# Kernel optimization log

Measured on AMD Instinct MI355X. Metric: run time of the kernel, lower is better.

Reference implementation:

```python
import jax, jax.numpy as jnp
import numpy as np

ALPHA = 0.2  # LeakyReLU negative slope
EPS = 1e-16


def setup_inputs() -> dict:
    key = jax.random.key(0)
    k0, k1, k2, k3 = jax.random.split(key, 4)
    N, E, F_in, F_out, HEADS = 50000, 1600000, 256, 128, 4
    H = jax.random.normal(k0, (N, F_in), dtype=jnp.float32)
    edge_index = jax.random.randint(k1, (2, E), 0, N)  # row0=src, row1=dst
    # Xavier-ish scaled params
    W = jax.random.normal(k2, (HEADS, F_out, F_in), dtype=jnp.float32) * (1.0 / np.sqrt(F_in))
    a = jax.random.normal(k3, (HEADS, 2 * F_out), dtype=jnp.float32) * 0.1
    bias = jnp.zeros((F_out,), dtype=jnp.float32)
    return {"H": H, "edge_index": edge_index, "W": W, "a": a, "bias": bias}


def reference(H, edge_index, W, a, bias):
    """GAT layer: per-head edge attention + segment softmax over src + SpMM, mean over heads.

    H: [N, F_in]; edge_index: [2, E]; W: [heads, F_out, F_in]; a: [heads, 2*F_out]; bias: [F_out]
    Note: a(concat(h_src, h_dst)) == h_src @ a[:F_out] + h_dst @ a[F_out:], so we compute the
    two per-node scores once on nodes instead of materializing the E x 2*F_out concat.
    """
    N = H.shape[0]
    heads, F_out, _ = W.shape
    src, dst = edge_index[0], edge_index[1]
    outs = []
    for h in range(heads):
        Ht = H @ W[h].T                      # [N, F_out]
        s_src = Ht @ a[h, :F_out]            # [N]
        s_dst = Ht @ a[h, F_out:]            # [N]
        e = s_src[src] + s_dst[dst]          # [E]
        e = jnp.where(e > 0, e, ALPHA * e)   # LeakyReLU
        # segment softmax over src nodes (matches scatter amax + scatter_add)
        e_max = jax.ops.segment_max(e, src, num_segments=N)    # [N], -inf for isolated nodes
        e_exp = jnp.exp(e - e_max[src])                         # [E]
        denom = jax.ops.segment_sum(e_exp, src, num_segments=N) # [N]
        attn = e_exp / (denom[src] + EPS)                       # [E]
        # sparse.mm(attention, Ht): out[i] = sum_{(i,j) in E} attn_ij * Ht[j]
        out = jax.ops.segment_sum(attn[:, None] * Ht[dst], src, num_segments=N)  # [N, F_out]
        outs.append(out)
    final = jnp.mean(jnp.stack(outs, axis=0), axis=0) + bias
    return final
```

## Files before the change

### kernel.cpp

```cpp
#include <hip/hip_runtime.h>

#define ALPHA 0.2f
#define EPS 1e-16f

static constexpr int F_IN = 256;
static constexpr int F_OUT = 128;
static constexpr int HEADS = 4;
static constexpr int COLS = HEADS * F_OUT;

typedef __bf16 bf16x8 __attribute__((ext_vector_type(8)));
typedef float f32x4 __attribute__((ext_vector_type(4)));

static __device__ __forceinline__ unsigned short f2bf(float f) {
  unsigned int u = __float_as_uint(f);
  unsigned int r = (u + 0x7FFFu + ((u >> 16) & 1u)) >> 16;
  return (unsigned short)r;
}
static __device__ __forceinline__ float bf_lo(unsigned int u) {
  return __uint_as_float(u << 16);
}
static __device__ __forceinline__ float bf_hi(unsigned int u) {
  return __uint_as_float(u & 0xFFFF0000u);
}
static __device__ __forceinline__ void cvt8(const float4& p0, const float4& p1, bf16x8& v) {
  v[0] = (__bf16)p0.x; v[1] = (__bf16)p0.y; v[2] = (__bf16)p0.z; v[3] = (__bf16)p0.w;
  v[4] = (__bf16)p1.x; v[5] = (__bf16)p1.y; v[6] = (__bf16)p1.z; v[7] = (__bf16)p1.w;
}

__global__ __launch_bounds__(256) void k_gemm_q(const float* __restrict__ A,
                                                const float* __restrict__ Wf,
                                                unsigned char* __restrict__ Hq,
                                                unsigned char* __restrict__ rec,
                                                float* __restrict__ ssrc,
                                                const float* __restrict__ Av, int N, int Tg,
                                                const int* __restrict__ src,
                                                int* __restrict__ cnt,
                                                unsigned short* __restrict__ rank, int E) {
  if ((int)blockIdx.x >= Tg) {
    int i = ((int)blockIdx.x - Tg) * 256 + threadIdx.x;
    const int stride = 1024 * 256;
    for (; i < E; i += stride) rank[i] = (unsigned short)atomicAdd(&cnt[src[i]], 1);
    return;
  }
  __shared__ __bf16 As[128][40];
  __shared__ __bf16 Bs[128][40];
  __shared__ float sS[128], sD[128];
  const int q8 = Tg >> 3, r8 = Tg & 7;
  const int xcd = blockIdx.x & 7, ii = blockIdx.x >> 3;
  const int gp = (xcd < r8) ? xcd * (q8 + 1) + ii
                            : r8 * (q8 + 1) + (xcd - r8) * q8 + ii;
  const int by = gp >> 2;
  const int bx = gp & 3;
  const int t = threadIdx.x;
  const int w = t >> 6, l = t & 63;
  const int wr = w >> 1, wc = w & 1;
  const int m0 = by << 7, n0 = bx << 7;
  const int lr = t >> 1, seg16 = (t & 1) << 4;
  int ar = m0 + lr; if (ar >= N) ar = N - 1;
  const float* Ap = A + (size_t)ar * F_IN + seg16;
  const float* Wp = Wf + (size_t)(n0 + lr) * F_IN + seg16;
  f32x4 acc[4][4] = {};
  for (int k0 = 0; k0 < F_IN; k0 += 32) {
    const float4 f0 = *(const float4*)(Ap + k0);
    const float4 f1 = *(const float4*)(Ap + k0 + 4);
    const float4 f2 = *(const float4*)(Ap + k0 + 8);
    const float4 f3 = *(const float4*)(Ap + k0 + 12);
    const float4 g0 = *(const float4*)(Wp + k0);
    const float4 g1 = *(const float4*)(Wp + k0 + 4);
    const float4 g2 = *(const float4*)(Wp + k0 + 8);
    const float4 g3 = *(const float4*)(Wp + k0 + 12);
    bf16x8 v0, v1, u0, u1;
    cvt8(f0, f1, v0); cvt8(f2, f3, v1);
    cvt8(g0, g1, u0); cvt8(g2, g3, u1);
    __syncthreads();
    *(bf16x8*)&As[lr][seg16] = v0;  *(bf16x8*)&As[lr][seg16 + 8] = v1;
    *(bf16x8*)&Bs[lr][seg16] = u0;  *(bf16x8*)&Bs[lr][seg16 + 8] = u1;
    __syncthreads();
    const int kb = (l >> 4) << 3;
    bf16x8 af[4], bf_[4];
#pragma unroll
    for (int mi = 0; mi < 4; ++mi)
      af[mi] = *(const bf16x8*)&As[(wr << 6) + (mi << 4) + (l & 15)][kb];
#pragma unroll
    for (int ni = 0; ni < 4; ++ni)
      bf_[ni] = *(const bf16x8*)&Bs[(wc << 6) + (ni << 4) + (l & 15)][kb];
#pragma unroll
    for (int mi = 0; mi < 4; ++mi)
#pragma unroll
      for (int ni = 0; ni < 4; ++ni)
        acc[mi][ni] = __builtin_amdgcn_mfma_f32_16x16x32_bf16(af[mi], bf_[ni], acc[mi][ni], 0, 0, 0);
  }
  {
    float as_[4], ad_[4];
#pragma unroll
    for (int ni = 0; ni < 4; ++ni) {
      const int f = (wc << 6) + (ni << 4) + (l & 15);
      as_[ni] = Av[bx * 256 + f];
      ad_[ni] = Av[bx * 256 + 128 + f];
    }
#pragma unroll
    for (int mi = 0; mi < 4; ++mi)
#pragma unroll
      for (int r = 0; r < 4; ++r) {
        float ds_ = 0.f, dd_ = 0.f;
#pragma unroll
        for (int ni = 0; ni < 4; ++ni) {
          ds_ = fmaf(acc[mi][ni][r], as_[ni], ds_);
          dd_ = fmaf(acc[mi][ni][r], ad_[ni], dd_);
        }
#pragma unroll
        for (int m = 1; m < 16; m <<= 1) {
          ds_ += __shfl_xor(ds_, m);
          dd_ += __shfl_xor(dd_, m);
        }
        if (wc == 0 && (l & 15) == 0) {
          const int rl = (wr << 6) + (mi << 4) + ((l >> 4) << 2) + r;
          sS[rl] = ds_; sD[rl] = dd_;
        }
      }
    __syncthreads();
    if (wc == 1) {
#pragma unroll
      for (int mi = 0; mi < 4; ++mi)
#pragma unroll
        for (int r = 0; r < 4; ++r) {
          float ds_ = 0.f, dd_ = 0.f;
#pragma unroll
          for (int ni = 0; ni < 4; ++ni) {
            ds_ = fmaf(acc[mi][ni][r], as_[ni], ds_);
            dd_ = fmaf(acc[mi][ni][r], ad_[ni], dd_);
          }
#pragma unroll
          for (int m = 1; m < 16; m <<= 1) {
            ds_ += __shfl_xor(ds_, m);
            dd_ += __shfl_xor(dd_, m);
          }
          if ((l & 15) == 0) {
            const int rl = (wr << 6) + (mi << 4) + ((l >> 4) << 2) + r;
            const int row = m0 + rl;
            if (row < N) {
              ssrc[row * 4 + bx] = sS[rl] + ds_;
              *(float*)&rec[(size_t)row * 32 + (bx << 2)] = sD[rl] + dd_;
            }
          }
        }
    }
  }
  const int bxg = (bx << 1) + wc;
#pragma unroll
  for (int mi = 0; mi < 4; ++mi)
#pragma unroll
    for (int r = 0; r < 4; ++r) {
      float mx = 0.f;
#pragma unroll
      for (int ni = 0; ni < 4; ++ni) mx = fmaxf(mx, fabsf(acc[mi][ni][r]));
#pragma unroll
      for (int m = 1; m < 16; m <<= 1) mx = fmaxf(mx, __shfl_xor(mx, m));
      const int row = m0 + (wr << 6) + (mi << 4) + ((l >> 4) << 2) + r;
      if (row < N) {
        const float inv = (mx > 0.f) ? 127.f / mx : 0.f;
        if ((l & 15) == 0)
          *(unsigned short*)&rec[(size_t)row * 32 + 16 + (bxg << 1)] = f2bf(mx * (1.f / 127.f));
        unsigned int pk = 0;
#pragma unroll
        for (int ni = 0; ni < 4; ++ni) {
          float tq = fminf(fmaxf(rintf(acc[mi][ni][r] * inv), -127.f), 127.f);
          pk |= ((unsigned int)(((int)tq + 128) & 255)) << (8 * ni);
        }
        *(unsigned int*)&Hq[(size_t)row * 512 + (bxg << 6) + ((l & 15) << 2)] = pk;
      }
    }
}

__global__ __launch_bounds__(1024) void k_scan1(int* __restrict__ cnt,
                                                int* __restrict__ bsum, int N) {
  __shared__ int ws[16];
  const int t = threadIdx.x, g = blockIdx.x * 1024 + t;
  const int lane = t & 63, w = t >> 6;
  int v = (g < N) ? cnt[g] : 0;
#pragma unroll
  for (int o = 1; o < 64; o <<= 1) {
    const int y = __shfl_up(v, o);
    if (lane >= o) v += y;
  }
  if (lane == 63) ws[w] = v;
  __syncthreads();
  if (w == 0) {
    int s = (lane < 16) ? ws[lane] : 0;
#pragma unroll
    for (int o = 1; o < 16; o <<= 1) {
      const int y = __shfl_up(s, o);
      if (lane >= o) s += y;
    }
    if (lane < 16) ws[lane] = s;
  }
  __syncthreads();
  v += (w > 0) ? ws[w - 1] : 0;
  if (g < N) cnt[g] = v;
  if (t == 1023) bsum[blockIdx.x] = v;
}

__global__ __launch_bounds__(1024) void k_scan3(const int* __restrict__ part,
                                                const int* __restrict__ bsum,
                                                int* __restrict__ off, int N, int nb) {
  __shared__ int sbuf[256];
  const int t = threadIdx.x;
  if (t < 64) {
    int carry = 0;
    for (int base = 0; base < nb; base += 64) {
      int v = (base + t < nb) ? bsum[base + t] : 0;
#pragma unroll
      for (int o = 1; o < 64; o <<= 1) {
        const int y = __shfl_up(v, o);
        if (t >= o) v += y;
      }
      v += carry;
      if (base + t < nb) sbuf[base + t] = v;
      carry = __shfl(v, 63);
    }
  }
  __syncthreads();
  const int g = blockIdx.x * 1024 + t;
  if (g == 0) off[0] = 0;
  if (g < N) off[g + 1] = part[g] + (blockIdx.x ? sbuf[blockIdx.x - 1] : 0);
}

__global__ void k_scatter(const int* __restrict__ src, const int* __restrict__ dst,
                          const int* __restrict__ off, const unsigned short* __restrict__ rank,
                          unsigned short* __restrict__ csr_dst, int E) {
  int i = blockIdx.x * blockDim.x + threadIdx.x;
  const int stride = gridDim.x * blockDim.x;
  for (; i < E; i += stride)
    csr_dst[off[src[i]] + rank[i]] = (unsigned short)dst[i];
}

__global__ __launch_bounds__(256) void k_spmm(const uint2* __restrict__ Hq2,
    const float4* __restrict__ ssrc4, const unsigned char* __restrict__ rec,
    const int* __restrict__ off, const unsigned short* __restrict__ csr_dst,
    const float* __restrict__ bias, float* __restrict__ out, int N) {
  __shared__ float wbuf[4][8][72];
  __shared__ int   ibuf[4][64];
  const int wv = threadIdx.x >> 6;
  const int lane = threadIdx.x & 63;
  const int n = (blockIdx.x << 2) + wv;
  if (n >= N) return;
  const int hg = lane >> 4;
  const int b8 = lane >> 3;
  const float4 ss4 = ssrc4[n];
  float den4[4] = {};
  float acc[8] = {};
  float sw = 0.f;
  const int beg = off[n], end = off[n + 1];
  for (int c0 = beg; c0 < end; c0 += 64) {
    const int cnt = min(64, end - c0);
    if (lane < cnt) {
      const int d = csr_dst[c0 + lane];
      ibuf[wv][lane] = d << 6;
      const float4 sd4 = *(const float4*)&rec[(size_t)d * 32];
      const uint4  sc  = *(const uint4*)&rec[(size_t)d * 32 + 16];
      float e0 = ss4.x + sd4.x; e0 = fmaxf(e0, ALPHA * e0);
      float e1 = ss4.y + sd4.y; e1 = fmaxf(e1, ALPHA * e1);
      float e2 = ss4.z + sd4.z; e2 = fmaxf(e2, ALPHA * e2);
      float e3 = ss4.w + sd4.w; e3 = fmaxf(e3, ALPHA * e3);
      const float w0 = __expf(e0), w1 = __expf(e1), w2 = __expf(e2), w3 = __expf(e3);
      den4[0] += w0; den4[1] += w1; den4[2] += w2; den4[3] += w3;
      wbuf[wv][0][lane] = w0 * bf_lo(sc.x); wbuf[wv][1][lane] = w0 * bf_hi(sc.x);
      wbuf[wv][2][lane] = w1 * bf_lo(sc.y); wbuf[wv][3][lane] = w1 * bf_hi(sc.y);
      wbuf[wv][4][lane] = w2 * bf_lo(sc.z); wbuf[wv][5][lane] = w2 * bf_hi(sc.z);
      wbuf[wv][6][lane] = w3 * bf_lo(sc.w); wbuf[wv][7][lane] = w3 * bf_hi(sc.w);
    }
#pragma unroll 8
    for (int j = 0; j < cnt; ++j) {
      const float wgt = wbuf[wv][b8][j];
      const int db = ibuf[wv][j];
      const uint2 q = Hq2[db + lane];
      sw += wgt;
      acc[0] = fmaf(wgt, (float)(q.x & 0xffu),         acc[0]);
      acc[1] = fmaf(wgt, (float)((q.x >> 8) & 0xffu),  acc[1]);
      acc[2] = fmaf(wgt, (float)((q.x >> 16) & 0xffu), acc[2]);
      acc[3] = fmaf(wgt, (float)(q.x >> 24),           acc[3]);
      acc[4] = fmaf(wgt, (float)(q.y & 0xffu),         acc[4]);
      acc[5] = fmaf(wgt, (float)((q.y >> 8) & 0xffu),  acc[5]);
      acc[6] = fmaf(wgt, (float)((q.y >> 16) & 0xffu), acc[6]);
      acc[7] = fmaf(wgt, (float)(q.y >> 24),           acc[7]);
    }
  }
#pragma unroll
  for (int k = 0; k < 4; ++k)
#pragma unroll
    for (int m = 1; m < 64; m <<= 1) den4[k] += __shfl_xor(den4[k], m);
  const float r = 1.f / (den4[hg] + EPS);
  const float corr = 128.f * sw;
#pragma unroll
  for (int i = 0; i < 8; ++i) acc[i] = (acc[i] - corr) * r;
#pragma unroll
  for (int i = 0; i < 8; ++i) {
    acc[i] += __shfl_xor(acc[i], 16);
    acc[i] += __shfl_xor(acc[i], 32);
  }
  if (lane < 16) {
    const int base = ((lane >> 3) & 1) * 64 + ((lane & 7) << 1);
#pragma unroll
    for (int k = 0; k < 4; ++k) {
      const float2 b2 = *(const float2*)&bias[base + k * 16];
      *(float2*)&out[(size_t)n * F_OUT + base + k * 16] =
          make_float2(0.25f * acc[k] + b2.x, 0.25f * acc[k + 4] + b2.y);
    }
  }
}

extern "C" void kernel_launch(void* const* d_in, const int* in_sizes, int n_in,
                              void* d_out, int out_size, void* d_ws, size_t ws_size,
                              hipStream_t stream) {
  const float* H    = (const float*)d_in[0];
  const int*   ei   = (const int*)d_in[1];
  const float* W    = (const float*)d_in[2];
  const float* a    = (const float*)d_in[3];
  const float* bias = (const float*)d_in[4];
  const int N = in_sizes[0] / F_IN;
  const int E = in_sizes[1] / 2;
  const int* src = ei;
  const int* dst = ei + E;

  char* ws = (char*)d_ws;
  size_t o = 0;
  auto alloc = [&](size_t bytes) -> void* {
    void* p = ws + o;
    o = (o + bytes + 255) & ~(size_t)255;
    return p;
  };
  unsigned char*  Hq  = (unsigned char*)alloc((size_t)N * COLS);
  float* ssrc = (float*)alloc((size_t)N * HEADS * sizeof(float));
  unsigned char* rec = (unsigned char*)alloc((size_t)N * 32);
  int*   cnt  = (int*)alloc((size_t)N * sizeof(int));
  int*   off  = (int*)alloc(((size_t)N + 1) * sizeof(int));
  unsigned short* csr = (unsigned short*)alloc((size_t)E * sizeof(unsigned short));
  unsigned short* rank = (unsigned short*)alloc((size_t)E * sizeof(unsigned short));
  const int nb = (N + 1023) / 1024;
  int*   bsum = (int*)alloc((size_t)nb * sizeof(int));

  hipMemsetAsync(cnt, 0, (size_t)N * sizeof(int), stream);

  const int nb128 = (N + 127) / 128;
  const int Tg = 4 * nb128;
  k_gemm_q<<<Tg + 1024, 256, 0, stream>>>(H, W, Hq, rec, ssrc, a, N, Tg,
                                          src, cnt, rank, E);
  k_scan1<<<nb, 1024, 0, stream>>>(cnt, bsum, N);
  k_scan3<<<nb, 1024, 0, stream>>>(cnt, bsum, off, N, nb);
  k_scatter<<<1024, 256, 0, stream>>>(src, dst, off, rank, csr, E);
  k_spmm<<<(N + 3) / 4, 256, 0, stream>>>((const uint2*)Hq, (const float4*)ssrc,
                                          rec, off, csr, bias, (float*)d_out, N);
}
```

Measured before the change: 290.1 us.

## Replace global-atomic CSR build with LDS-binned counting split across GEMM-overlapped launches

Global atomics used for per-edge rank counting are replaced by LDS-binned histograms: 64 edge chunks × 4 source ranges, with 16-bit packed counters. A per-chunk base-offset table is built, and a placement kernel then assigns CSR slots using LDS atomics. The GEMM tiles are split into four slices, and each slice is co-launched with one CSR-build phase (histogram, local scan, block scan, base computation) so the GEMM hides that latency. This drops the memset, the rank array and the scattered global atomics. In exchange it adds bcnt/base tables of size 64×N, extra passes over src, and a 16-bit per-bin count limit.

```diff
diff --git a/kernel.cpp b/kernel.cpp
--- a/kernel.cpp
+++ b/kernel.cpp
@@ -7,6 +7,7 @@
 static constexpr int F_OUT = 128;
 static constexpr int HEADS = 4;
 static constexpr int COLS = HEADS * F_OUT;
+static constexpr int NCH = 64;
 
 typedef __bf16 bf16x8 __attribute__((ext_vector_type(8)));
 typedef float f32x4 __attribute__((ext_vector_type(4)));
@@ -27,99 +28,75 @@
   v[4] = (__bf16)p1.x; v[5] = (__bf16)p1.y; v[6] = (__bf16)p1.z; v[7] = (__bf16)p1.w;
 }
 
-__global__ __launch_bounds__(256) void k_gemm_q(const float* __restrict__ A,
-                                                const float* __restrict__ Wf,
-                                                unsigned char* __restrict__ Hq,
-                                                unsigned char* __restrict__ rec,
-                                                float* __restrict__ ssrc,
-                                                const float* __restrict__ Av, int N, int Tg,
-                                                const int* __restrict__ src,
-                                                int* __restrict__ cnt,
-                                                unsigned short* __restrict__ rank, int E) {
-  if ((int)blockIdx.x >= Tg) {
-    int i = ((int)blockIdx.x - Tg) * 256 + threadIdx.x;
-    const int stride = 1024 * 256;
-    for (; i < E; i += stride) rank[i] = (unsigned short)atomicAdd(&cnt[src[i]], 1);
-    return;
-  }
-  __shared__ __bf16 As[128][40];
-  __shared__ __bf16 Bs[128][40];
-  __shared__ float sS[128], sD[128];
-  const int q8 = Tg >> 3, r8 = Tg & 7;
-  const int xcd = blockIdx.x & 7, ii = blockIdx.x >> 3;
-  const int gp = (xcd < r8) ? xcd * (q8 + 1) + ii
-                            : r8 * (q8 + 1) + (xcd - r8) * q8 + ii;
-  const int by = gp >> 2;
-  const int bx = gp & 3;
+__global__ __launch_bounds__(256) void k_merged(int mode, int Cb, int start, int len,
+    const float* __restrict__ A, const float* __restrict__ Wf,
+    unsigned char* __restrict__ Hq, unsigned char* __restrict__ rec,
+    float* __restrict__ ssrc, const float* __restrict__ Av, int N,
+    const int* __restrict__ src, unsigned short* __restrict__ bcnt,
+    int* __restrict__ cnt, int* __restrict__ bsum, int* __restrict__ off,
+    unsigned int* __restrict__ base32, int E, int RNG, int Npad, int nscan) {
+  __shared__ union {
+    unsigned int bins[6272];
+    struct { __bf16 As[128][40]; __bf16 Bs[128][40]; float sS[128]; float sD[128]; } g;
+    int ws[4];
+    int sbuf[256];
+  } u;
   const int t = threadIdx.x;
-  const int w = t >> 6, l = t & 63;
-  const int wr = w >> 1, wc = w & 1;
-  const int m0 = by << 7, n0 = bx << 7;
-  const int lr = t >> 1, seg16 = (t & 1) << 4;
-  int ar = m0 + lr; if (ar >= N) ar = N - 1;
-  const float* Ap = A + (size_t)ar * F_IN + seg16;
-  const float* Wp = Wf + (size_t)(n0 + lr) * F_IN + seg16;
-  f32x4 acc[4][4] = {};
-  for (int k0 = 0; k0 < F_IN; k0 += 32) {
-    const float4 f0 = *(const float4*)(Ap + k0);
-    const float4 f1 = *(const float4*)(Ap + k0 + 4);
-    const float4 f2 = *(const float4*)(Ap + k0 + 8);
-    const float4 f3 = *(const float4*)(Ap + k0 + 12);
-    const float4 g0 = *(const float4*)(Wp + k0);
-    const float4 g1 = *(const float4*)(Wp + k0 + 4);
-    const float4 g2 = *(const float4*)(Wp + k0 + 8);
-    const float4 g3 = *(const float4*)(Wp + k0 + 12);
-    bf16x8 v0, v1, u0, u1;
-    cvt8(f0, f1, v0); cvt8(f2, f3, v1);
-    cvt8(g0, g1, u0); cvt8(g2, g3, u1);
-    __syncthreads();
-    *(bf16x8*)&As[lr][seg16] = v0;  *(bf16x8*)&As[lr][seg16 + 8] = v1;
-    *(bf16x8*)&Bs[lr][seg16] = u0;  *(bf16x8*)&Bs[lr][seg16 + 8] = u1;
-    __syncthreads();
-    const int kb = (l >> 4) << 3;
-    bf16x8 af[4], bf_[4];
-#pragma unroll
-    for (int mi = 0; mi < 4; ++mi)
-      af[mi] = *(const bf16x8*)&As[(wr << 6) + (mi << 4) + (l & 15)][kb];
-#pragma unroll
-    for (int ni = 0; ni < 4; ++ni)
-      bf_[ni] = *(const bf16x8*)&Bs[(wc << 6) + (ni << 4) + (l & 15)][kb];
-#pragma unroll
-    for (int mi = 0; mi < 4; ++mi)
+
+  if ((int)blockIdx.x >= Cb) {
+    const int j = (int)blockIdx.x - Cb;
+    const int q8 = len >> 3, r8 = len & 7;
+    const int x = j & 7, ii = j >> 3;
+    const int p = start + ((x < r8) ? x * (q8 + 1) + ii
+                                    : r8 * (q8 + 1) + (x - r8) * q8 + ii);
+    const int by = p >> 2;
+    const int bx = p & 3;
+    const int w = t >> 6, l = t & 63;
+    const int wr = w >> 1, wc = w & 1;
+    const int m0 = by << 7, n0 = bx << 7;
+    const int lr = t >> 1, seg16 = (t & 1) << 4;
+    int ar = m0 + lr; if (ar >= N) ar = N - 1;
+    const float* Ap = A + (size_t)ar * F_IN + seg16;
+    const float* Wp = Wf + (size_t)(n0 + lr) * F_IN + seg16;
+    f32x4 acc[4][4] = {};
+    for (int k0 = 0; k0 < F_IN; k0 += 32) {
+      const float4 f0 = *(const float4*)(Ap + k0);
+      const float4 f1 = *(const float4*)(Ap + k0 + 4);
+      const float4 f2 = *(const float4*)(Ap + k0 + 8);
+      const float4 f3 = *(const float4*)(Ap + k0 + 12);
+      const float4 g0 = *(const float4*)(Wp + k0);
+      const float4 g1 = *(const float4*)(Wp + k0 + 4);
+      const float4 g2 = *(const float4*)(Wp + k0 + 8);
+      const float4 g3 = *(const float4*)(Wp + k0 + 12);
+      bf16x8 v0, v1, u0, u1;
+      cvt8(f0, f1, v0); cvt8(f2, f3, v1);
+      cvt8(g0, g1, u0); cvt8(g2, g3, u1);
+      __syncthreads();
+      *(bf16x8*)&u.g.As[lr][seg16] = v0;  *(bf16x8*)&u.g.As[lr][seg16 + 8] = v1;
+      *(bf16x8*)&u.g.Bs[lr][seg16] = u0;  *(bf16x8*)&u.g.Bs[lr][seg16 + 8] = u1;
+      __syncthreads();
+      const int kb = (l >> 4) << 3;
+      bf16x8 af[4], bf_[4];
+#pragma unroll
+      for (int mi = 0; mi < 4; ++mi)
+        af[mi] = *(const bf16x8*)&u.g.As[(wr << 6) + (mi << 4) + (l & 15)][kb];
 #pragma unroll
       for (int ni = 0; ni < 4; ++ni)
-        acc[mi][ni] = __builtin_amdgcn_mfma_f32_16x16x32_bf16(af[mi], bf_[ni], acc[mi][ni], 0, 0, 0);
-  }
-  {
-    float as_[4], ad_[4];
-#pragma unroll
-    for (int ni = 0; ni < 4; ++ni) {
-      const int f = (wc << 6) + (ni << 4) + (l & 15);
-      as_[ni] = Av[bx * 256 + f];
-      ad_[ni] = Av[bx * 256 + 128 + f];
-    }
-#pragma unroll
-    for (int mi = 0; mi < 4; ++mi)
-#pragma unroll
-      for (int r = 0; r < 4; ++r) {
-        float ds_ = 0.f, dd_ = 0.f;
-#pragma unroll
-        for (int ni = 0; ni < 4; ++ni) {
-          ds_ = fmaf(acc[mi][ni][r], as_[ni], ds_);
-          dd_ = fmaf(acc[mi][ni][r], ad_[ni], dd_);
-        }
-#pragma unroll
-        for (int m = 1; m < 16; m <<= 1) {
-          ds_ += __shfl_xor(ds_, m);
-          dd_ += __shfl_xor(dd_, m);
-        }
-        if (wc == 0 && (l & 15) == 0) {
-          const int rl = (wr << 6) + (mi << 4) + ((l >> 4) << 2) + r;
-          sS[rl] = ds_; sD[rl] = dd_;
-        }
+        bf_[ni] = *(const bf16x8*)&u.g.Bs[(wc << 6) + (ni << 4) + (l & 15)][kb];
+#pragma unroll
+      for (int mi = 0; mi < 4; ++mi)
+#pragma unroll
+        for (int ni = 0; ni < 4; ++ni)
+          acc[mi][ni] = __builtin_amdgcn_mfma_f32_16x16x32_bf16(af[mi], bf_[ni], acc[mi][ni], 0, 0, 0);
+    }
+    {
+      float as_[4], ad_[4];
+#pragma unroll
+      for (int ni = 0; ni < 4; ++ni) {
+        const int f = (wc << 6) + (ni << 4) + (l & 15);
+        as_[ni] = Av[bx * 256 + f];
+        ad_[ni] = Av[bx * 256 + 128 + f];
       }
-    __syncthreads();
-    if (wc == 1) {
 #pragma unroll
       for (int mi = 0; mi < 4; ++mi)
 #pragma unroll
@@ -135,103 +112,164 @@
             ds_ += __shfl_xor(ds_, m);
             dd_ += __shfl_xor(dd_, m);
           }
-          if ((l & 15) == 0) {
+          if (wc == 0 && (l & 15) == 0) {
             const int rl = (wr << 6) + (mi << 4) + ((l >> 4) << 2) + r;
-            const int row = m0 + rl;
-            if (row < N) {
-              ssrc[row * 4 + bx] = sS[rl] + ds_;
-              *(float*)&rec[(size_t)row * 32 + (bx << 2)] = sD[rl] + dd_;
+            u.g.sS[rl] = ds_; u.g.sD[rl] = dd_;
+          }
+        }
+      __syncthreads();
+      if (wc == 1) {
+#pragma unroll
+        for (int mi = 0; mi < 4; ++mi)
+#pragma unroll
+          for (int r = 0; r < 4; ++r) {
+            float ds_ = 0.f, dd_ = 0.f;
+#pragma unroll
+            for (int ni = 0; ni < 4; ++ni) {
+              ds_ = fmaf(acc[mi][ni][r], as_[ni], ds_);
+              dd_ = fmaf(acc[mi][ni][r], ad_[ni], dd_);
+            }
+#pragma unroll
+            for (int m = 1; m < 16; m <<= 1) {
+              ds_ += __shfl_xor(ds_, m);
+              dd_ += __shfl_xor(dd_, m);
+            }
+            if ((l & 15) == 0) {
+              const int rl = (wr << 6) + (mi << 4) + ((l >> 4) << 2) + r;
+              const int row = m0 + rl;
+              if (row < N) {
+                ssrc[row * 4 + bx] = u.g.sS[rl] + ds_;
+                *(float*)&rec[(size_t)row * 32 + (bx << 2)] = u.g.sD[rl] + dd_;
+              }
             }
           }
+      }
+    }
+    const int bxg = (bx << 1) + wc;
+#pragma unroll
+    for (int mi = 0; mi < 4; ++mi)
+#pragma unroll
+      for (int r = 0; r < 4; ++r) {
+        float mx = 0.f;
+#pragma unroll
+        for (int ni = 0; ni < 4; ++ni) mx = fmaxf(mx, fabsf(acc[mi][ni][r]));
+#pragma unroll
+        for (int m = 1; m < 16; m <<= 1) mx = fmaxf(mx, __shfl_xor(mx, m));
+        const int row = m0 + (wr << 6) + (mi << 4) + ((l >> 4) << 2) + r;
+        if (row < N) {
+          const float inv = (mx > 0.f) ? 127.f / mx : 0.f;
+          if ((l & 15) == 0)
+            *(unsigned short*)&rec[(size_t)row * 32 + 16 + (bxg << 1)] = f2bf(mx * (1.f / 127.f));
+          unsigned int pk = 0;
+#pragma unroll
+          for (int ni = 0; ni < 4; ++ni) {
+            float tq = fminf(fmaxf(rintf(acc[mi][ni][r] * inv), -127.f), 127.f);
+            pk |= ((unsigned int)(((int)tq + 128) & 255)) << (8 * ni);
+          }
+          *(unsigned int*)&Hq[(size_t)row * 512 + (bxg << 6) + ((l & 15) << 2)] = pk;
         }
-    }
-  }
-  const int bxg = (bx << 1) + wc;
-#pragma unroll
-  for (int mi = 0; mi < 4; ++mi)
-#pragma unroll
-    for (int r = 0; r < 4; ++r) {
-      float mx = 0.f;
-#pragma unroll
-      for (int ni = 0; ni < 4; ++ni) mx = fmaxf(mx, fabsf(acc[mi][ni][r]));
-#pragma unroll
-      for (int m = 1; m < 16; m <<= 1) mx = fmaxf(mx, __shfl_xor(mx, m));
-      const int row = m0 + (wr << 6) + (mi << 4) + ((l >> 4) << 2) + r;
-      if (row < N) {
-        const float inv = (mx > 0.f) ? 127.f / mx : 0.f;
-        if ((l & 15) == 0)
-          *(unsigned short*)&rec[(size_t)row * 32 + 16 + (bxg << 1)] = f2bf(mx * (1.f / 127.f));
-        unsigned int pk = 0;
-#pragma unroll
-        for (int ni = 0; ni < 4; ++ni) {
-          float tq = fminf(fmaxf(rintf(acc[mi][ni][r] * inv), -127.f), 127.f);
-          pk |= ((unsigned int)(((int)tq + 128) & 255)) << (8 * ni);
+      }
+    return;
+  }
+
+  if (mode == 0) {
+    const int ec = blockIdx.x & (NCH - 1), rq = blockIdx.x >> 6;
+    const int r0 = rq * RNG;
+    const int nw = RNG >> 1;
+    for (int jj = t; jj < nw; jj += 256) u.bins[jj] = 0u;
+    __syncthreads();
+    const int CE = (E + NCH - 1) / NCH;
+    const int i0 = ec * CE, i1 = min(E, i0 + CE);
+    for (int i = i0 + t; i < i1; i += 256) {
+      const unsigned us = (unsigned)(src[i] - r0);
+      if (us < (unsigned)RNG) atomicAdd(&u.bins[us >> 1], 1u << ((us & 1) << 4));
+    }
+    __syncthreads();
+    uint4* dv = (uint4*)(bcnt + (size_t)ec * Npad + r0);
+    const uint4* sv = (const uint4*)u.bins;
+    const int nv = RNG >> 3;
+    for (int m = t; m < nv; m += 256) dv[m] = sv[m];
+  } else if (mode == 1) {
+    const int g = blockIdx.x * 256 + t;
+    const int lane = t & 63, w = t >> 6;
+    int v = 0;
+    if (g < N) {
+#pragma unroll 8
+      for (int b = 0; b < NCH; ++b) v += bcnt[(size_t)b * Npad + g];
+    }
+#pragma unroll
+    for (int o = 1; o < 64; o <<= 1) {
+      const int y = __shfl_up(v, o);
+      if (lane >= o) v += y;
+    }
+    if (lane == 63) u.ws[w] = v;
+    __syncthreads();
+    if (t == 0) {
+      int s = 0;
+#pragma unroll
+      for (int k = 0; k < 4; ++k) { s += u.ws[k]; u.ws[k] = s; }
+    }
+    __syncthreads();
+    v += (w > 0) ? u.ws[w - 1] : 0;
+    if (g < N) cnt[g] = v;
+    if (t == 255) bsum[blockIdx.x] = v;
+  } else if (mode == 2) {
+    if (t < 64) {
+      int carry = 0;
+      for (int base = 0; base < nscan; base += 64) {
+        int v = (base + t < nscan) ? bsum[base + t] : 0;
+#pragma unroll
+        for (int o = 1; o < 64; o <<= 1) {
+          const int y = __shfl_up(v, o);
+          if (t >= o) v += y;
         }
-        *(unsigned int*)&Hq[(size_t)row * 512 + (bxg << 6) + ((l & 15) << 2)] = pk;
+        v += carry;
+        if (base + t < nscan) u.sbuf[base + t] = v;
+        carry = __shfl(v, 63);
       }
     }
-}
-
-__global__ __launch_bounds__(1024) void k_scan1(int* __restrict__ cnt,
-                                                int* __restrict__ bsum, int N) {
-  __shared__ int ws[16];
-  const int t = threadIdx.x, g = blockIdx.x * 1024 + t;
-  const int lane = t & 63, w = t >> 6;
-  int v = (g < N) ? cnt[g] : 0;
-#pragma unroll
-  for (int o = 1; o < 64; o <<= 1) {
-    const int y = __shfl_up(v, o);
-    if (lane >= o) v += y;
-  }
-  if (lane == 63) ws[w] = v;
+    __syncthreads();
+    const int g = blockIdx.x * 256 + t;
+    if (g == 0) off[0] = 0;
+    if (g < N) off[g + 1] = cnt[g] + (blockIdx.x ? u.sbuf[blockIdx.x - 1] : 0);
+  } else {
+    const int s = blockIdx.x * 256 + t;
+    if (s < N) {
+      unsigned int run = (unsigned int)off[s];
+#pragma unroll 8
+      for (int b = 0; b < NCH; ++b) {
+        const size_t idx = (size_t)b * Npad + s;
+        const unsigned int v = bcnt[idx];
+        base32[idx] = run;
+        run += v;
+      }
+    }
+  }
+}
+
+__global__ __launch_bounds__(256) void k_place(const int* __restrict__ src,
+                                               const int* __restrict__ dst,
+                                               const unsigned int* __restrict__ base32,
+                                               unsigned short* __restrict__ csr,
+                                               int E, int RNG, int Npad) {
+  __shared__ unsigned int bins[6272];
+  const int ec = blockIdx.x & (NCH - 1), rq = blockIdx.x >> 6;
+  const int r0 = rq * RNG, t = threadIdx.x;
+  const int nw = RNG >> 1;
+  for (int jj = t; jj < nw; jj += 256) bins[jj] = 0u;
   __syncthreads();
-  if (w == 0) {
-    int s = (lane < 16) ? ws[lane] : 0;
-#pragma unroll
-    for (int o = 1; o < 16; o <<= 1) {
-      const int y = __shfl_up(s, o);
-      if (lane >= o) s += y;
-    }
-    if (lane < 16) ws[lane] = s;
-  }
-  __syncthreads();
-  v += (w > 0) ? ws[w - 1] : 0;
-  if (g < N) cnt[g] = v;
-  if (t == 1023) bsum[blockIdx.x] = v;
-}
-
-__global__ __launch_bounds__(1024) void k_scan3(const int* __restrict__ part,
-                                                const int* __restrict__ bsum,
-                                                int* __restrict__ off, int N, int nb) {
-  __shared__ int sbuf[256];
-  const int t = threadIdx.x;
-  if (t < 64) {
-    int carry = 0;
-    for (int base = 0; base < nb; base += 64) {
-      int v = (base + t < nb) ? bsum[base + t] : 0;
-#pragma unroll
-      for (int o = 1; o < 64; o <<= 1) {
-        const int y = __shfl_up(v, o);
-        if (t >= o) v += y;
-      }
-      v += carry;
-      if (base + t < nb) sbuf[base + t] = v;
-      carry = __shfl(v, 63);
-    }
-  }
-  __syncthreads();
-  const int g = blockIdx.x * 1024 + t;
-  if (g == 0) off[0] = 0;
-  if (g < N) off[g + 1] = part[g] + (blockIdx.x ? sbuf[blockIdx.x - 1] : 0);
-}
-
-__global__ void k_scatter(const int* __restrict__ src, const int* __restrict__ dst,
-                          const int* __restrict__ off, const unsigned short* __restrict__ rank,
-                          unsigned short* __restrict__ csr_dst, int E) {
-  int i = blockIdx.x * blockDim.x + threadIdx.x;
-  const int stride = gridDim.x * blockDim.x;
-  for (; i < E; i += stride)
-    csr_dst[off[src[i]] + rank[i]] = (unsigned short)dst[i];
+  const unsigned int* brow = base32 + (size_t)ec * Npad;
+  const int CE = (E + NCH - 1) / NCH;
+  const int i0 = ec * CE, i1 = min(E, i0 + CE);
+  for (int i = i0 + t; i < i1; i += 256) {
+    const int s = src[i];
+    const unsigned us = (unsigned)(s - r0);
+    if (us < (unsigned)RNG) {
+      const unsigned int old = atomicAdd(&bins[us >> 1], 1u << ((us & 1) << 4));
+      const int local = (old >> ((us & 1) << 4)) & 0xffff;
+      csr[brow[s] + local] = (unsigned short)dst[i];
+    }
+  }
 }
 
 __global__ __launch_bounds__(256) void k_spmm(const uint2* __restrict__ Hq2,
@@ -322,6 +360,10 @@
   const int* src = ei;
   const int* dst = ei + E;
 
+  const int RNG  = ((((N + 3) >> 2) + 7) & ~7);
+  const int Npad = RNG * 4;
+  const int nscan = (N + 255) / 256;
+
   char* ws = (char*)d_ws;
   size_t o = 0;
   auto alloc = [&](size_t bytes) -> void* {
@@ -334,20 +376,26 @@
   unsigned char* rec = (unsigned char*)alloc((size_t)N * 32);
   int*   cnt  = (int*)alloc((size_t)N * sizeof(int));
   int*   off  = (int*)alloc(((size_t)N + 1) * sizeof(int));
-  unsigned short* csr = (unsigned short*)alloc((size_t)E * sizeof(unsigned short));
-  unsigned short* rank = (unsigned short*)alloc((size_t)E * sizeof(unsigned short));
-  const int nb = (N + 1023) / 1024;
-  int*   bsum = (int*)alloc((size_t)nb * sizeof(int));
-
-  hipMemsetAsync(cnt, 0, (size_t)N * sizeof(int), stream);
-
-  const int nb128 = (N + 127) / 128;
-  const int Tg = 4 * nb128;
-  k_gemm_q<<<Tg + 1024, 256, 0, stream>>>(H, W, Hq, rec, ssrc, a, N, Tg,
-                                          src, cnt, rank, E);
-  k_scan1<<<nb, 1024, 0, stream>>>(cnt, bsum, N);
-  k_scan3<<<nb, 1024, 0, stream>>>(cnt, bsum, off, N, nb);
-  k_scatter<<<1024, 256, 0, stream>>>(src, dst, off, rank, csr, E);
+  unsigned short* csr  = (unsigned short*)alloc((size_t)E * sizeof(unsigned short));
+  unsigned short* bcnt = (unsigned short*)alloc((size_t)NCH * Npad * 2);
+  unsigned int*  base  = (unsigned int*)alloc((size_t)NCH * Npad * 4);
+  int*   bsum = (int*)alloc((size_t)nscan * sizeof(int));
+
+  const int Tg = 4 * ((N + 127) / 128);
+  const int c0 = (Tg + 3) / 4;
+  const int starts[4] = {0, c0, 2 * c0, 3 * c0};
+  const int lens[4]   = {c0, c0, c0, Tg - 3 * c0};
+
+  k_merged<<<256 + lens[0], 256, 0, stream>>>(0, 256, starts[0], lens[0],
+      H, W, Hq, rec, ssrc, a, N, src, bcnt, cnt, bsum, off, base, E, RNG, Npad, nscan);
+  k_merged<<<nscan + lens[1], 256, 0, stream>>>(1, nscan, starts[1], lens[1],
+      H, W, Hq, rec, ssrc, a, N, src, bcnt, cnt, bsum, off, base, E, RNG, Npad, nscan);
+  k_merged<<<nscan + lens[2], 256, 0, stream>>>(2, nscan, starts[2], lens[2],
+      H, W, Hq, rec, ssrc, a, N, src, bcnt, cnt, bsum, off, base, E, RNG, Npad, nscan);
+  k_merged<<<nscan + lens[3], 256, 0, stream>>>(3, nscan, starts[3], lens[3],
+      H, W, Hq, rec, ssrc, a, N, src, bcnt, cnt, bsum, off, base, E, RNG, Npad, nscan);
+
+  k_place<<<256, 256, 0, stream>>>(src, dst, base, csr, E, RNG, Npad);
   k_spmm<<<(N + 3) / 4, 256, 0, stream>>>((const uint2*)Hq, (const float4*)ssrc,
                                           rec, off, csr, bias, (float*)d_out, N);
 }
```

After: 323.2 us. 1.11x slower.
